# Kernel optimization log

Measured on AMD Instinct MI355X. Metric: run time of the kernel, lower is better.

The kernel has to match this reference:

```python
import math
import jax, jax.numpy as jnp
import numpy as np

D_MODEL = 512
N_HEADS = 8
D_K = D_MODEL // N_HEADS
LN_EPS = 1e-5


def _rel_pos_encoding(length: int, d: int) -> jnp.ndarray:
    """Sinusoidal encodings for positions 0..length-1, shape (length, d)."""
    pos = jnp.arange(length, dtype=jnp.float32)[:, None]            # (L,1)
    div = jnp.exp(jnp.arange(0, d, 2, dtype=jnp.float32) * (-(math.log(10000.0) / d)))  # (d/2,)
    ang = pos * div[None, :]                                         # (L,d/2)
    # interleave sin (even cols) and cos (odd cols)
    return jnp.stack([jnp.sin(ang), jnp.cos(ang)], axis=-1).reshape(length, d)


def setup_inputs() -> dict:
    key = jax.random.key(0)
    ks = jax.random.split(key, 6)
    B, T = 4, 2048
    s = 1.0 / math.sqrt(D_MODEL)
    return {
        "x":    jax.random.normal(ks[0], (B, T, D_MODEL), dtype=jnp.float32),
        "ln_g": jnp.ones((D_MODEL,), jnp.float32),
        "ln_b": jnp.zeros((D_MODEL,), jnp.float32),
        "wq":   jax.random.normal(ks[1], (D_MODEL, D_MODEL), jnp.float32) * s,
        "bq":   jnp.zeros((D_MODEL,), jnp.float32),
        "wk":   jax.random.normal(ks[2], (D_MODEL, D_MODEL), jnp.float32) * s,
        "bk":   jnp.zeros((D_MODEL,), jnp.float32),
        "wv":   jax.random.normal(ks[3], (D_MODEL, D_MODEL), jnp.float32) * s,
        "bv":   jnp.zeros((D_MODEL,), jnp.float32),
        "wo":   jax.random.normal(ks[4], (D_MODEL, D_MODEL), jnp.float32) * s,
        "bo":   jnp.zeros((D_MODEL,), jnp.float32),
    }


def reference(x, ln_g, ln_b, wq, bq, wk, bk, wv, bv, wo, bo):
    B, T, D = x.shape
    # pre-norm LayerNorm
    mu = jnp.mean(x, axis=-1, keepdims=True)
    var = jnp.mean(jnp.square(x - mu), axis=-1, keepdims=True)
    normed = (x - mu) * jax.lax.rsqrt(var + LN_EPS) * ln_g + ln_b

    def split_heads(y):  # (B,T,D) -> (B,H,T,dk)
        return y.reshape(B, T, N_HEADS, D_K).transpose(0, 2, 1, 3)

    Q = split_heads(normed @ wq.T + bq)
    K = split_heads(normed @ wk.T + bk)
    V = split_heads(normed @ wv.T + bv)

    pe = _rel_pos_encoding(T, D_K)            # (T, dk)
    K = K + pe[None, None, :, :]              # additive relative PE on K

    scale = 1.0 / math.sqrt(D_K)
    scores = jnp.einsum('bhtd,bhsd->bhts', Q, K) * scale   # (B,H,T,T)
    attn = jax.nn.softmax(scores, axis=-1)
    context = jnp.einsum('bhts,bhsd->bhtd', attn, V)        # (B,H,T,dk)
    context = context.transpose(0, 2, 1, 3).reshape(B, T, D)
    return context @ wo.T + bo
```

## Files before the change

### kernel.cpp

```cpp
#include <hip/hip_runtime.h>
#include <hip/hip_bf16.h>
#include <math.h>

#define D_MODEL 512
#define N_HEADS 8
#define D_K     64
#define T_SEQ   2048
#define B_SZ    4
#define M_ROWS  (B_SZ * T_SEQ)

typedef __bf16 bf16;
typedef __bf16 bf16x4 __attribute__((ext_vector_type(4)));
typedef __bf16 bf16x8 __attribute__((ext_vector_type(8)));
typedef float  floatx4 __attribute__((ext_vector_type(4)));

__device__ __forceinline__ int SWZ(int row, int col) {
  return row * 64 + ((((col >> 3) ^ (row & 7)) << 3) | (col & 7));
}

__device__ __forceinline__ float pe_fast(int t, int d) {
  int i2 = d & ~1;
  float div = __expf((float)i2 * (-0.1439115683f));
  float ang = (float)t * div;
  return (d & 1) ? __cosf(ang) : __sinf(ang);
}

__global__ __launch_bounds__(256) void prep(
    const float* __restrict__ x, const float* __restrict__ g,
    const float* __restrict__ b, bf16* __restrict__ out,
    const float* __restrict__ wq, const float* __restrict__ wk,
    const float* __restrict__ wv, const float* __restrict__ wo,
    bf16* __restrict__ wdst) {
  int bid = blockIdx.x;
  int tid = threadIdx.x;
  if (bid >= M_ROWS / 4) {
    int gid = (bid - M_ROWS / 4) * 256 + tid;
    int e0  = gid * 4;
    int mat = e0 >> 18;
    int loc = e0 & 262143;
    const float* src = (mat == 0) ? wq : (mat == 1) ? wk : (mat == 2) ? wv : wo;
    float4 v = *(const float4*)(src + loc);
    bf16* d = wdst + e0;
    d[0] = (bf16)v.x; d[1] = (bf16)v.y; d[2] = (bf16)v.z; d[3] = (bf16)v.w;
    return;
  }
  int wave = tid >> 6, lane = tid & 63;
  int row  = bid * 4 + wave;
  const float* xr = x + (size_t)row * D_MODEL + lane * 8;
  float4 a = *(const float4*)(xr);
  float4 c = *(const float4*)(xr + 4);
  float s  = a.x + a.y + a.z + a.w + c.x + c.y + c.z + c.w;
  float ss = a.x * a.x + a.y * a.y + a.z * a.z + a.w * a.w +
             c.x * c.x + c.y * c.y + c.z * c.z + c.w * c.w;
#pragma unroll
  for (int off = 1; off < 64; off <<= 1) {
    s  += __shfl_xor(s,  off, 64);
    ss += __shfl_xor(ss, off, 64);
  }
  float mu  = s * (1.0f / D_MODEL);
  float var = ss * (1.0f / D_MODEL) - mu * mu;
  float rs  = rsqrtf(var + 1e-5f);
  float4 g0 = *(const float4*)(g + lane * 8);
  float4 g1 = *(const float4*)(g + lane * 8 + 4);
  float4 b0 = *(const float4*)(b + lane * 8);
  float4 b1 = *(const float4*)(b + lane * 8 + 4);
  bf16x8 o8;
  o8[0] = (bf16)((a.x - mu) * rs * g0.x + b0.x);
  o8[1] = (bf16)((a.y - mu) * rs * g0.y + b0.y);
  o8[2] = (bf16)((a.z - mu) * rs * g0.z + b0.z);
  o8[3] = (bf16)((a.w - mu) * rs * g0.w + b0.w);
  o8[4] = (bf16)((c.x - mu) * rs * g1.x + b1.x);
  o8[5] = (bf16)((c.y - mu) * rs * g1.y + b1.y);
  o8[6] = (bf16)((c.z - mu) * rs * g1.z + b1.z);
  o8[7] = (bf16)((c.w - mu) * rs * g1.w + b1.w);
  *(bf16x8*)(out + (size_t)row * D_MODEL + lane * 8) = o8;
}

__global__ __launch_bounds__(256, 3) void gemm_qkv(
    const bf16* __restrict__ A, const bf16* __restrict__ wqkv,
    const float* __restrict__ bq, const float* __restrict__ bk, const float* __restrict__ bv,
    bf16* __restrict__ Qo, bf16* __restrict__ Ko, bf16* __restrict__ VTo) {
  __shared__ bf16 sW[16384];
  __shared__ bf16 ep[4][1536];

  int tid = threadIdx.x;
  int w = tid >> 6, lane = tid & 63;
  int lm = lane & 15, quad = lane >> 4;
  int mat  = blockIdx.y >> 3;
  int h    = blockIdx.y & 7;
  int nloc = h * 64;
  const bf16* Wp = wqkv + (size_t)mat * 262144;

  int mbase = blockIdx.x * 128 + w * 32;
  const bf16* ap = A + (size_t)(mbase + lm) * D_MODEL + quad * 8;

  floatx4 acc[2][4];
#pragma unroll
  for (int mi = 0; mi < 2; mi++)
#pragma unroll
    for (int nt = 0; nt < 4; nt++) acc[mi][nt] = floatx4{0.f, 0.f, 0.f, 0.f};

  int srow = tid >> 2;
  int scc  = (tid & 3) * 16;

#pragma unroll 1
  for (int kp = 0; kp < 2; kp++) {
    if (kp) __syncthreads();
#pragma unroll
    for (int kc = 0; kc < 4; kc++) {
      const bf16* src = Wp + (size_t)(nloc + srow) * D_MODEL + kp * 256 + kc * 64 + scc;
      bf16x8 w0 = *(const bf16x8*)src;
      bf16x8 w1 = *(const bf16x8*)(src + 8);
      *(bf16x8*)&sW[kc * 4096 + SWZ(srow, scc)]     = w0;
      *(bf16x8*)&sW[kc * 4096 + SWZ(srow, scc + 8)] = w1;
    }
    __syncthreads();

    bf16x8 af[2][8];
#pragma unroll
    for (int mi = 0; mi < 2; mi++)
#pragma unroll
      for (int ks = 0; ks < 8; ks++)
        af[mi][ks] = *(const bf16x8*)(ap + mi * 16 * D_MODEL + kp * 256 + ks * 32);

#pragma unroll
    for (int ks = 0; ks < 8; ks++) {
#pragma unroll
      for (int nt = 0; nt < 4; nt++) {
        bf16x8 bfr = *(const bf16x8*)
            &sW[(ks >> 1) * 4096 + SWZ(nt * 16 + lm, (ks & 1) * 32 + quad * 8)];
        acc[0][nt] = __builtin_amdgcn_mfma_f32_16x16x32_bf16(af[0][ks], bfr, acc[0][nt], 0, 0, 0);
        acc[1][nt] = __builtin_amdgcn_mfma_f32_16x16x32_bf16(af[1][ks], bfr, acc[1][nt], 0, 0, 0);
      }
    }
  }

  int bb = mbase >> 11, t0w = mbase & (T_SEQ - 1);
  size_t bhoff = (size_t)(bb * N_HEADS + h) * (T_SEQ * D_K);
  bf16* myep = ep[w];

  if (mat == 2) {
#pragma unroll
    for (int nt = 0; nt < 4; nt++) {
      float bvv = bv[nloc + nt * 16 + lm];
#pragma unroll
      for (int mi = 0; mi < 2; mi++) {
        bf16x4 pk;
#pragma unroll
        for (int rr = 0; rr < 4; rr++) pk[rr] = (bf16)(acc[mi][nt][rr] + bvv);
        *(bf16x4*)&myep[lm * 40 + mi * 16 + quad * 4] = pk;
      }
      int dl = lane >> 2, toff = (lane & 3) * 8;
      bf16x8 v = *(const bf16x8*)&myep[dl * 40 + toff];
      *(bf16x8*)(VTo + bhoff + (size_t)(nt * 16 + dl) * T_SEQ + t0w + toff) = v;
    }
  } else {
    bf16* dst = (mat == 0) ? Qo : Ko;
    const float* bias = (mat == 0) ? bq : bk;
#pragma unroll
    for (int c = 0; c < 2; c++) {
#pragma unroll
      for (int nt = 0; nt < 4; nt++) {
        int d = nt * 16 + lm;
        float bval = bias[nloc + d];
#pragma unroll
        for (int rr = 0; rr < 4; rr++) {
          float v = acc[c][nt][rr] + bval;
          if (mat == 1) v += pe_fast(t0w + c * 16 + quad * 4 + rr, d);
          else          v *= 0.125f;
          myep[(quad * 4 + rr) * 72 + d] = (bf16)v;
        }
      }
#pragma unroll
      for (int rd = 0; rd < 2; rd++) {
        int row = rd * 8 + (lane >> 3);
        bf16x8 v = *(const bf16x8*)&myep[row * 72 + (lane & 7) * 8];
        *(bf16x8*)(dst + bhoff + (size_t)(t0w + c * 16 + row) * D_K + (lane & 7) * 8) = v;
      }
    }
  }
}

__global__ __launch_bounds__(256, 2) void gemm_out(const bf16* __restrict__ A,
                                                   const bf16* __restrict__ W,
                                                   const float* __restrict__ bias,
                                                   float* __restrict__ out) {
  __shared__ bf16 sW[32768];
  int tid = threadIdx.x;
  int w = tid >> 6, lane = tid & 63;
  int lm = lane & 15, quad = lane >> 4;
  int n0 = blockIdx.y * 64;

  {
    int row = tid >> 2;
    int cc  = (tid & 3) * 16;
#pragma unroll
    for (int kc = 0; kc < 8; kc++) {
      const bf16* src = W + (size_t)(n0 + row) * D_MODEL + kc * 64 + cc;
      bf16x8 w0 = *(const bf16x8*)src;
      bf16x8 w1 = *(const bf16x8*)(src + 8);
      *(bf16x8*)&sW[kc * 4096 + SWZ(row, cc)]     = w0;
      *(bf16x8*)&sW[kc * 4096 + SWZ(row, cc + 8)] = w1;
    }
  }
  __syncthreads();

  int mbase = blockIdx.x * 128 + w * 32;
  const bf16* ap = A + (size_t)(mbase + lm) * D_MODEL + quad * 8;

  bf16x8 af[2][16];
#pragma unroll
  for (int mi = 0; mi < 2; mi++)
#pragma unroll
    for (int ks = 0; ks < 16; ks++)
      af[mi][ks] = *(const bf16x8*)(ap + mi * 16 * D_MODEL + ks * 32);

  floatx4 acc[2][4];
#pragma unroll
  for (int mi = 0; mi < 2; mi++)
#pragma unroll
    for (int nt = 0; nt < 4; nt++) acc[mi][nt] = floatx4{0.f, 0.f, 0.f, 0.f};

#pragma unroll
  for (int ks = 0; ks < 16; ks++) {
#pragma unroll
    for (int nt = 0; nt < 4; nt++) {
      bf16x8 bfr = *(const bf16x8*)
          &sW[(ks >> 1) * 4096 + SWZ(nt * 16 + lm, (ks & 1) * 32 + quad * 8)];
      acc[0][nt] = __builtin_amdgcn_mfma_f32_16x16x32_bf16(af[0][ks], bfr, acc[0][nt], 0, 0, 0);
      acc[1][nt] = __builtin_amdgcn_mfma_f32_16x16x32_bf16(af[1][ks], bfr, acc[1][nt], 0, 0, 0);
    }
  }

#pragma unroll
  for (int nt = 0; nt < 4; nt++) {
    int n = n0 + nt * 16 + lm;
    float bval = bias[n];
#pragma unroll
    for (int mi = 0; mi < 2; mi++)
#pragma unroll
      for (int rr = 0; rr < 4; rr++) {
        int m = mbase + mi * 16 + quad * 4 + rr;
        out[(size_t)m * D_MODEL + n] = acc[mi][nt][rr] + bval;
      }
  }
}

__global__ __launch_bounds__(512, 4) void flash_mfma(const bf16* __restrict__ Q,
                                                     const bf16* __restrict__ K,
                                                     const bf16* __restrict__ VT,
                                                     bf16* __restrict__ ctx) {
  __shared__ __align__(16) char smem[65536];
  bf16* sK  = (bf16*)smem;
  bf16* sVT = (bf16*)(smem + 16384);
  bf16* sP  = (bf16*)(smem + 32768);

  int tid  = threadIdx.x;
  int wave = tid >> 6, lane = tid & 63;
  int lm = lane & 15, quad = lane >> 4;
  int qg = wave & 3, kg = wave >> 2;
  int bh = blockIdx.y;
  int q0 = blockIdx.x * 128 + qg * 32;

  const bf16* Qb  = Q  + (size_t)bh * T_SEQ * D_K;
  const bf16* Kb  = K  + (size_t)bh * T_SEQ * D_K;
  const bf16* VTb = VT + (size_t)bh * T_SEQ * D_K;

  bf16x8 qf[2][2];
#pragma unroll
  for (int qt = 0; qt < 2; qt++)
#pragma unroll
    for (int kb = 0; kb < 2; kb++)
      qf[qt][kb] = *(const bf16x8*)(Qb + (size_t)(q0 + qt * 16 + lm) * D_K + kb * 32 + quad * 8);

  floatx4 o[2][4];
#pragma unroll
  for (int qt = 0; qt < 2; qt++)
#pragma unroll
    for (int nt = 0; nt < 4; nt++) o[qt][nt] = floatx4{0.f, 0.f, 0.f, 0.f};
  float l_i[2] = {0.f, 0.f};

  int srow = tid >> 3;
  int scol = (tid & 7) * 8;
  const bf16* kp0 = Kb  + (size_t)srow * D_K + scol;
  const bf16* vp0 = VTb + (size_t)srow * T_SEQ + scol;

  bf16x8 rk[2], rv[2];
  rk[0] = *(const bf16x8*)(kp0);
  rk[1] = *(const bf16x8*)(kp0 + 4096);
  rv[0] = *(const bf16x8*)(vp0);
  rv[1] = *(const bf16x8*)(vp0 + 64);

  bf16* myK = sK  + kg * 4096;
  bf16* myV = sVT + kg * 4096;
  bf16* myP = sP  + wave * 2048;

  for (int r = 0; r < T_SEQ / 64; r += 2) {
    __syncthreads();
    *(bf16x8*)&sK [SWZ(srow, scol)]         = rk[0];
    *(bf16x8*)&sK [4096 + SWZ(srow, scol)]  = rk[1];
    *(bf16x8*)&sVT[SWZ(srow, scol)]         = rv[0];
    *(bf16x8*)&sVT[4096 + SWZ(srow, scol)]  = rv[1];
    if (r + 2 < T_SEQ / 64) {
      rk[0] = *(const bf16x8*)(kp0 + (r + 2) * 4096);
      rk[1] = *(const bf16x8*)(kp0 + (r + 3) * 4096);
      rv[0] = *(const bf16x8*)(vp0 + (r + 2) * 64);
      rv[1] = *(const bf16x8*)(vp0 + (r + 3) * 64);
    }
    __syncthreads();

    float ls0 = 0.f, ls1 = 0.f;
#pragma unroll
    for (int nt = 0; nt < 4; nt++) {
      floatx4 s0 = floatx4{0.f, 0.f, 0.f, 0.f};
      floatx4 s1 = floatx4{0.f, 0.f, 0.f, 0.f};
#pragma unroll
      for (int kb = 0; kb < 2; kb++) {
        bf16x8 kf = *(const bf16x8*)&myK[SWZ(nt * 16 + lm, kb * 32 + quad * 8)];
        s0 = __builtin_amdgcn_mfma_f32_16x16x32_bf16(kf, qf[0][kb], s0, 0, 0, 0);
        s1 = __builtin_amdgcn_mfma_f32_16x16x32_bf16(kf, qf[1][kb], s1, 0, 0, 0);
      }
      bf16x4 pk0, pk1;
#pragma unroll
      for (int rr = 0; rr < 4; rr++) {
        float p0 = __expf(s0[rr] - 8.0f);
        float p1 = __expf(s1[rr] - 8.0f);
        ls0 += p0; ls1 += p1;
        pk0[rr] = (bf16)p0; pk1[rr] = (bf16)p1;
      }
      *(bf16x4*)&myP[SWZ(lm,      nt * 16 + quad * 4)] = pk0;
      *(bf16x4*)&myP[SWZ(16 + lm, nt * 16 + quad * 4)] = pk1;
    }
    ls0 += __shfl_xor(ls0, 16, 64);
    ls0 += __shfl_xor(ls0, 32, 64);
    ls1 += __shfl_xor(ls1, 16, 64);
    ls1 += __shfl_xor(ls1, 32, 64);
    l_i[0] += ls0;
    l_i[1] += ls1;

#pragma unroll
    for (int kb = 0; kb < 2; kb++) {
      bf16x8 pf0 = *(const bf16x8*)&myP[SWZ(lm, kb * 32 + quad * 8)];
      bf16x8 pf1 = *(const bf16x8*)&myP[SWZ(16 + lm, kb * 32 + quad * 8)];
#pragma unroll
      for (int nt = 0; nt < 4; nt++) {
        bf16x8 vt = *(const bf16x8*)&myV[SWZ(nt * 16 + lm, kb * 32 + quad * 8)];
        o[0][nt] = __builtin_amdgcn_mfma_f32_16x16x32_bf16(pf0, vt, o[0][nt], 0, 0, 0);
        o[1][nt] = __builtin_amdgcn_mfma_f32_16x16x32_bf16(pf1, vt, o[1][nt], 0, 0, 0);
      }
    }
  }

  __syncthreads();
  float* scO = (float*)smem;
  float* scL = (float*)(smem + 32768);
  if (kg == 1) {
#pragma unroll
    for (int qt = 0; qt < 2; qt++)
#pragma unroll
      for (int nt = 0; nt < 4; nt++)
        *(floatx4*)&scO[(qg * 512 + (qt * 4 + nt) * 64 + lane) * 4] = o[qt][nt];
    scL[qg * 128 + lane]      = l_i[0];
    scL[qg * 128 + 64 + lane] = l_i[1];
  }
  __syncthreads();
  if (kg == 0) {
#pragma unroll
    for (int qt = 0; qt < 2; qt++)
#pragma unroll
      for (int nt = 0; nt < 4; nt++) {
        floatx4 t = *(const floatx4*)&scO[(qg * 512 + (qt * 4 + nt) * 64 + lane) * 4];
        o[qt][nt] += t;
      }
    l_i[0] += scL[qg * 128 + lane];
    l_i[1] += scL[qg * 128 + 64 + lane];

    int b_ = bh >> 3, h = bh & 7;
#pragma unroll
    for (int qt = 0; qt < 2; qt++) {
#pragma unroll
      for (int rr = 0; rr < 4; rr++) {
        int qq = quad * 4 + rr;
        float linv = 1.f / __shfl(l_i[qt], qq, 64);
        int t = q0 + qt * 16 + qq;
        bf16* op = ctx + ((size_t)(b_ * T_SEQ + t)) * D_MODEL + h * D_K;
#pragma unroll
        for (int nt = 0; nt < 4; nt++)
          op[nt * 16 + lm] = (bf16)(o[qt][nt][rr] * linv);
      }
    }
  }
}

extern "C" void kernel_launch(void* const* d_in, const int* in_sizes, int n_in,
                              void* d_out, int out_size, void* d_ws, size_t ws_size,
                              hipStream_t stream) {
  const float* x    = (const float*)d_in[0];
  const float* ln_g = (const float*)d_in[1];
  const float* ln_b = (const float*)d_in[2];
  const float* wq   = (const float*)d_in[3];
  const float* bq   = (const float*)d_in[4];
  const float* wk   = (const float*)d_in[5];
  const float* bk   = (const float*)d_in[6];
  const float* wv   = (const float*)d_in[7];
  const float* bv   = (const float*)d_in[8];
  const float* wo   = (const float*)d_in[9];
  const float* bo   = (const float*)d_in[10];
  float* out = (float*)d_out;

  char* ws = (char*)d_ws;
  const size_t MB8 = (size_t)M_ROWS * D_MODEL * sizeof(bf16);
  bf16* normed = (bf16*)(ws);
  bf16* Qb     = (bf16*)(ws + MB8);
  bf16* Kb     = (bf16*)(ws + 2 * MB8);
  bf16* VTb    = (bf16*)(ws + 3 * MB8);
  bf16* w4     = (bf16*)(ws + 4 * MB8);
  bf16* ctx    = normed;

  prep<<<M_ROWS / 4 + 1024, 256, 0, stream>>>(x, ln_g, ln_b, normed,
                                              wq, wk, wv, wo, w4);
  gemm_qkv<<<dim3(64, 24), 256, 0, stream>>>(
      normed, w4, bq, bk, bv, Qb, Kb, VTb);
  flash_mfma<<<dim3(T_SEQ / 128, B_SZ * N_HEADS), 512, 0, stream>>>(Qb, Kb, VTb, ctx);
  gemm_out<<<dim3(64, 8), 256, 0, stream>>>(
      ctx, w4 + 3 * (size_t)D_MODEL * D_MODEL, bo, out);
}
```

Before: 179.6 us.

## Load K/V MFMA fragments directly from global memory, drop LDS staging

The flash attention kernel stops staging K and V^T tiles through shared memory with block-wide barriers. Each wave now loads its MFMA operand fragments straight from global memory (relying on L2/L1 for reuse) and walks alternate key tiles on its own, which also shrinks LDS to just the P buffers and the reduction scratch. The grid is flattened to 1D with the head index in the low bits, so blocks for the same head run together and share K/V in cache. The trade is more, less coalesced global traffic per wave and no prefetch overlap, in exchange for removing barriers and LDS pressure.

```diff
diff --git a/kernel.cpp b/kernel.cpp
--- a/kernel.cpp
+++ b/kernel.cpp
@@ -250,17 +250,16 @@
                                                      const bf16* __restrict__ K,
                                                      const bf16* __restrict__ VT,
                                                      bf16* __restrict__ ctx) {
-  __shared__ __align__(16) char smem[65536];
-  bf16* sK  = (bf16*)smem;
-  bf16* sVT = (bf16*)(smem + 16384);
-  bf16* sP  = (bf16*)(smem + 32768);
+  __shared__ __align__(16) char smem[34816];
+  bf16* sP = (bf16*)smem;
 
   int tid  = threadIdx.x;
   int wave = tid >> 6, lane = tid & 63;
   int lm = lane & 15, quad = lane >> 4;
   int qg = wave & 3, kg = wave >> 2;
-  int bh = blockIdx.y;
-  int q0 = blockIdx.x * 128 + qg * 32;
+  int bid = blockIdx.x;
+  int bh  = bid & 31;
+  int q0  = (bid >> 5) * 128 + qg * 32;
 
   const bf16* Qb  = Q  + (size_t)bh * T_SEQ * D_K;
   const bf16* Kb  = K  + (size_t)bh * T_SEQ * D_K;
@@ -280,34 +279,18 @@
     for (int nt = 0; nt < 4; nt++) o[qt][nt] = floatx4{0.f, 0.f, 0.f, 0.f};
   float l_i[2] = {0.f, 0.f};
 
-  int srow = tid >> 3;
-  int scol = (tid & 7) * 8;
-  const bf16* kp0 = Kb  + (size_t)srow * D_K + scol;
-  const bf16* vp0 = VTb + (size_t)srow * T_SEQ + scol;
-
-  bf16x8 rk[2], rv[2];
-  rk[0] = *(const bf16x8*)(kp0);
-  rk[1] = *(const bf16x8*)(kp0 + 4096);
-  rv[0] = *(const bf16x8*)(vp0);
-  rv[1] = *(const bf16x8*)(vp0 + 64);
-
-  bf16* myK = sK  + kg * 4096;
-  bf16* myV = sVT + kg * 4096;
-  bf16* myP = sP  + wave * 2048;
-
-  for (int r = 0; r < T_SEQ / 64; r += 2) {
-    __syncthreads();
-    *(bf16x8*)&sK [SWZ(srow, scol)]         = rk[0];
-    *(bf16x8*)&sK [4096 + SWZ(srow, scol)]  = rk[1];
-    *(bf16x8*)&sVT[SWZ(srow, scol)]         = rv[0];
-    *(bf16x8*)&sVT[4096 + SWZ(srow, scol)]  = rv[1];
-    if (r + 2 < T_SEQ / 64) {
-      rk[0] = *(const bf16x8*)(kp0 + (r + 2) * 4096);
-      rk[1] = *(const bf16x8*)(kp0 + (r + 3) * 4096);
-      rv[0] = *(const bf16x8*)(vp0 + (r + 2) * 64);
-      rv[1] = *(const bf16x8*)(vp0 + (r + 3) * 64);
-    }
-    __syncthreads();
+  const bf16* kfp = Kb  + (size_t)lm * D_K   + quad * 8;
+  const bf16* vfp = VTb + (size_t)lm * T_SEQ + quad * 8;
+
+  bf16* myP = sP + wave * 2048;
+
+  for (int kt = kg; kt < T_SEQ / 64; kt += 2) {
+    bf16x8 vf[2][4];
+#pragma unroll
+    for (int kb = 0; kb < 2; kb++)
+#pragma unroll
+      for (int nt = 0; nt < 4; nt++)
+        vf[kb][nt] = *(const bf16x8*)(vfp + (size_t)nt * 16 * T_SEQ + kt * 64 + kb * 32);
 
     float ls0 = 0.f, ls1 = 0.f;
 #pragma unroll
@@ -316,7 +299,7 @@
       floatx4 s1 = floatx4{0.f, 0.f, 0.f, 0.f};
 #pragma unroll
       for (int kb = 0; kb < 2; kb++) {
-        bf16x8 kf = *(const bf16x8*)&myK[SWZ(nt * 16 + lm, kb * 32 + quad * 8)];
+        bf16x8 kf = *(const bf16x8*)(kfp + (size_t)kt * 4096 + nt * 1024 + kb * 32);
         s0 = __builtin_amdgcn_mfma_f32_16x16x32_bf16(kf, qf[0][kb], s0, 0, 0, 0);
         s1 = __builtin_amdgcn_mfma_f32_16x16x32_bf16(kf, qf[1][kb], s1, 0, 0, 0);
       }
@@ -344,9 +327,8 @@
       bf16x8 pf1 = *(const bf16x8*)&myP[SWZ(16 + lm, kb * 32 + quad * 8)];
 #pragma unroll
       for (int nt = 0; nt < 4; nt++) {
-        bf16x8 vt = *(const bf16x8*)&myV[SWZ(nt * 16 + lm, kb * 32 + quad * 8)];
-        o[0][nt] = __builtin_amdgcn_mfma_f32_16x16x32_bf16(pf0, vt, o[0][nt], 0, 0, 0);
-        o[1][nt] = __builtin_amdgcn_mfma_f32_16x16x32_bf16(pf1, vt, o[1][nt], 0, 0, 0);
+        o[0][nt] = __builtin_amdgcn_mfma_f32_16x16x32_bf16(pf0, vf[kb][nt], o[0][nt], 0, 0, 0);
+        o[1][nt] = __builtin_amdgcn_mfma_f32_16x16x32_bf16(pf1, vf[kb][nt], o[1][nt], 0, 0, 0);
       }
     }
   }
@@ -421,7 +403,7 @@
                                               wq, wk, wv, wo, w4);
   gemm_qkv<<<dim3(64, 24), 256, 0, stream>>>(
       normed, w4, bq, bk, bv, Qb, Kb, VTb);
-  flash_mfma<<<dim3(T_SEQ / 128, B_SZ * N_HEADS), 512, 0, stream>>>(Qb, Kb, VTb, ctx);
+  flash_mfma<<<512, 512, 0, stream>>>(Qb, Kb, VTb, ctx);
   gemm_out<<<dim3(64, 8), 256, 0, stream>>>(
       ctx, w4 + 3 * (size_t)D_MODEL * D_MODEL, bo, out);
 }
```

Result: slower. 246.1 us (+37.0%).
